# Kernel tuning notes

Hardware: AMD Instinct MI355X
Metric: run time of the kernel (lower is better)

## Reference

```python
import jax, jax.numpy as jnp
import numpy as np
from jax import lax

B, CIN, H, W = 2, 512, 64, 64
NCLS = 5
CI = CIN // 4      # inter_channels = 128
CQ = CI // 8       # PAM query/key channels = 16
EPS = 1e-5


def setup_inputs() -> dict:
    key = jax.random.key(0)
    it = iter(jax.random.split(key, 48))

    def nrm(shape, s=0.05):
        return jax.random.normal(next(it), shape, jnp.float32) * s

    def bn(c):
        w = jax.random.uniform(next(it), (c,), jnp.float32, 0.5, 1.5)
        b = nrm((c,))
        m = nrm((c,))
        v = jax.random.uniform(next(it), (c,), jnp.float32, 0.5, 1.5)
        return w, b, m, v

    inp = {}
    inp['x'] = jax.random.normal(next(it), (B, CIN, H, W), jnp.float32)
    inp['bn_a_w'], inp['bn_a_b'], inp['bn_a_m'], inp['bn_a_v'] = bn(CIN)
    inp['conv_a_w'] = nrm((CI, CIN, 3, 3))
    inp['bn_c_w'], inp['bn_c_b'], inp['bn_c_m'], inp['bn_c_v'] = bn(CIN)
    inp['conv_c_w'] = nrm((CI, CIN, 3, 3))
    inp['pam_q_w'] = nrm((CQ, CI)); inp['pam_q_b'] = nrm((CQ,))
    inp['pam_k_w'] = nrm((CQ, CI)); inp['pam_k_b'] = nrm((CQ,))
    inp['pam_v_w'] = nrm((CI, CI)); inp['pam_v_b'] = nrm((CI,))
    inp['pam_gamma'] = nrm((1,), 0.5)
    inp['cam_gamma'] = nrm((1,), 0.5)
    inp['bn_a1_w'], inp['bn_a1_b'], inp['bn_a1_m'], inp['bn_a1_v'] = bn(CI)
    inp['conv_a1_w'] = nrm((CIN, CI)); inp['conv_a1_b'] = nrm((CIN,))
    inp['bn_c1_w'], inp['bn_c1_b'], inp['bn_c1_m'], inp['bn_c1_v'] = bn(CI)
    inp['conv_c1_w'] = nrm((CIN, CI)); inp['conv_c1_b'] = nrm((CIN,))
    inp['out_a_w'] = nrm((NCLS, CIN)); inp['out_a_b'] = nrm((NCLS,))
    inp['out_c_w'] = nrm((NCLS, CIN)); inp['out_c_b'] = nrm((NCLS,))
    inp['out_f_w'] = nrm((NCLS, CIN)); inp['out_f_b'] = nrm((NCLS,))
    return inp


def _bn_relu(x, w, b, m, v):
    # eval-mode BatchNorm2d followed by ReLU
    scale = (w / jnp.sqrt(v + EPS))[None, :, None, None]
    shift = (b - m * w / jnp.sqrt(v + EPS))[None, :, None, None]
    return jax.nn.relu(x * scale + shift)


def _conv3(x, w):
    return lax.conv_general_dilated(x, w, (1, 1), 'SAME',
                                    dimension_numbers=('NCHW', 'OIHW', 'NCHW'))


def _conv1(x, w, b):
    # 1x1 conv as channel matmul
    return jnp.einsum('oi,bihw->bohw', w, x) + b[None, :, None, None]


def _pam(x, wq, bq, wk, bk, wv, bv, gamma):
    Bc, C, Hh, Ww = x.shape
    N = Hh * Ww
    q = _conv1(x, wq, bq).reshape(Bc, -1, N)   # [B,CQ,N]
    k = _conv1(x, wk, bk).reshape(Bc, -1, N)   # [B,CQ,N]
    v = _conv1(x, wv, bv).reshape(Bc, C, N)    # [B,C,N]
    energy = jnp.einsum('bcn,bcm->bnm', q, k)  # [B,N,N]
    attn = jax.nn.softmax(energy, axis=-1)
    out = jnp.einsum('bcm,bnm->bcn', v, attn).reshape(Bc, C, Hh, Ww)
    return gamma * out + x


def _cam(x, gamma):
    Bc, C, Hh, Ww = x.shape
    N = Hh * Ww
    f = x.reshape(Bc, C, N)
    energy = jnp.einsum('bcn,bdn->bcd', f, f)                    # [B,C,C]
    energy_new = jnp.max(energy, -1, keepdims=True) - energy
    attn = jax.nn.softmax(energy_new, axis=-1)
    out = jnp.einsum('bcd,bdn->bcn', attn, f).reshape(Bc, C, Hh, Ww)
    return gamma * out + x


def reference(x, bn_a_w, bn_a_b, bn_a_m, bn_a_v, conv_a_w,
              bn_c_w, bn_c_b, bn_c_m, bn_c_v, conv_c_w,
              pam_q_w, pam_q_b, pam_k_w, pam_k_b, pam_v_w, pam_v_b,
              pam_gamma, cam_gamma,
              bn_a1_w, bn_a1_b, bn_a1_m, bn_a1_v, conv_a1_w, conv_a1_b,
              bn_c1_w, bn_c1_b, bn_c1_m, bn_c1_v, conv_c1_w, conv_c1_b,
              out_a_w, out_a_b, out_c_w, out_c_b, out_f_w, out_f_b):
    # position-attention branch
    sa = _conv3(_bn_relu(x, bn_a_w, bn_a_b, bn_a_m, bn_a_v), conv_a_w)
    sa = _pam(sa, pam_q_w, pam_q_b, pam_k_w, pam_k_b, pam_v_w, pam_v_b, pam_gamma)
    sa = _conv1(_bn_relu(sa, bn_a1_w, bn_a1_b, bn_a1_m, bn_a1_v), conv_a1_w, conv_a1_b)
    # channel-attention branch
    sc = _conv3(_bn_relu(x, bn_c_w, bn_c_b, bn_c_m, bn_c_v), conv_c_w)
    sc = _cam(sc, cam_gamma)
    sc = _conv1(_bn_relu(sc, bn_c1_w, bn_c1_b, bn_c1_m, bn_c1_v), conv_c1_w, conv_c1_b)
    feat_fusion = sa + sc
    # dropout is identity at eval time
    sa_out = _conv1(sa, out_a_w, out_a_b)
    sc_out = _conv1(sc, out_c_w, out_c_b)
    sasc_out = _conv1(feat_fusion, out_f_w, out_f_b)
    return (feat_fusion, sasc_out, sa_out, sc_out)
```

## Files before the change

### kernel.cpp

```cpp
#include <hip/hip_runtime.h>

using u16 = unsigned short;
using short8 = __attribute__((ext_vector_type(8))) short;
using f32x4 = __attribute__((ext_vector_type(4))) float;

struct alignas(8) U16x4 { u16 x, y, z, w; };

__device__ __forceinline__ float bf2f(u16 u) {
  return __uint_as_float(((unsigned int)u) << 16);
}
__device__ __forceinline__ u16 f2bf(float f) {
  unsigned int u = __float_as_uint(f);
  unsigned int r = u + 0x7FFFu + ((u >> 16) & 1u);
  return (u16)(r >> 16);
}

__global__ void k_prep_w(const float* __restrict__ wa, const float* __restrict__ wc,
                         u16* __restrict__ Wb) {
  int idx = blockIdx.x * 256 + threadIdx.x;
  int j = idx & 7;
  int l = (idx >> 3) & 63;
  int ks = (idx >> 9) & 3;
  int rest = idx >> 11;
  int tap = rest % 9;
  int rest2 = rest / 9;
  int chunk = rest2 & 3;
  int mt = (rest2 >> 2) & 7;
  int br = rest2 >> 5;
  int co = mt * 16 + (l & 15);
  int ci = chunk * 128 + ks * 32 + (l >> 4) * 8 + j;
  const float* w = br ? wc : wa;
  Wb[idx] = f2bf(w[co * 4608 + ci * 9 + tap]);
}

__global__ void k_prep_w1(const float* __restrict__ wa, const float* __restrict__ wc,
                          u16* __restrict__ W1b) {
  int idx = blockIdx.x * 256 + threadIdx.x;
  int j = idx & 7;
  int l = (idx >> 3) & 63;
  int ks = (idx >> 9) & 3;
  int cot = (idx >> 11) & 31;
  int br = idx >> 16;
  int co = cot * 16 + (l & 15);
  int ci = ks * 32 + (l >> 4) * 8 + j;
  const float* w = br ? wc : wa;
  W1b[idx] = f2bf(w[co * 128 + ci]);
}

__global__ void k_prep_wqkv(const float* __restrict__ wq, const float* __restrict__ wk,
                            const float* __restrict__ wv, u16* __restrict__ Wq) {
  int idx = blockIdx.x * 256 + threadIdx.x;
  if (idx >= 20480) return;
  int j = idx & 7;
  int l = (idx >> 3) & 63;
  int ks = (idx >> 9) & 3;
  int cot = idx >> 11;
  int co = cot * 16 + (l & 15);
  int ci = ks * 32 + (l >> 4) * 8 + j;
  float w = co < 16 ? wq[co * 128 + ci]
          : (co < 32 ? wk[(co - 16) * 128 + ci] : wv[(co - 32) * 128 + ci]);
  Wq[idx] = f2bf(w);
}

__global__ __launch_bounds__(256) void k_bnrelu2t(const float* __restrict__ x,
    const float* __restrict__ wa, const float* __restrict__ ba,
    const float* __restrict__ ma, const float* __restrict__ va,
    const float* __restrict__ wc, const float* __restrict__ bc,
    const float* __restrict__ mc, const float* __restrict__ vc,
    u16* __restrict__ xa16, u16* __restrict__ xcb16) {
  __shared__ float sA[128], bA[128], sC[128], bC[128];
  __shared__ u16 ta[64 * 136], tc[64 * 136];
  int t = threadIdx.x;
  int h = blockIdx.x, b = blockIdx.y;
  int c0 = blockIdx.z * 128;
  if (t < 128) {
    int c = c0 + t;
    float s1 = wa[c] * rsqrtf(va[c] + 1e-5f);
    sA[t] = s1; bA[t] = ba[c] - ma[c] * s1;
    float s2 = wc[c] * rsqrtf(vc[c] + 1e-5f);
    sC[t] = s2; bC[t] = bc[c] - mc[c] * s2;
  }
  __syncthreads();
  const float* xb = x + ((size_t)b << 21) + (h << 6);
  u16* oa = xa16 + ((size_t)b << 21) + ((size_t)h << 15);
  u16* oc = xcb16 + ((size_t)b << 21) + ((size_t)h << 15);
  int w = t & 63, cg = t >> 6;
#pragma unroll
  for (int i = 0; i < 8; ++i) {
    int cl = cg * 4 + i * 16;
    int c = c0 + cl;
    const float* xp = xb + (size_t)c * 4096 + w;
    float v0 = xp[0], v1 = xp[4096], v2 = xp[8192], v3 = xp[12288];
    U16x4 pa, pc;
    pa.x = f2bf(fmaxf(fmaf(v0, sA[cl], bA[cl]), 0.f));
    pa.y = f2bf(fmaxf(fmaf(v1, sA[cl + 1], bA[cl + 1]), 0.f));
    pa.z = f2bf(fmaxf(fmaf(v2, sA[cl + 2], bA[cl + 2]), 0.f));
    pa.w = f2bf(fmaxf(fmaf(v3, sA[cl + 3], bA[cl + 3]), 0.f));
    pc.x = f2bf(fmaxf(fmaf(v0, sC[cl], bC[cl]), 0.f));
    pc.y = f2bf(fmaxf(fmaf(v1, sC[cl + 1], bC[cl + 1]), 0.f));
    pc.z = f2bf(fmaxf(fmaf(v2, sC[cl + 2], bC[cl + 2]), 0.f));
    pc.w = f2bf(fmaxf(fmaf(v3, sC[cl + 3], bC[cl + 3]), 0.f));
    *(U16x4*)(ta + w * 136 + cl) = pa;
    *(U16x4*)(tc + w * 136 + cl) = pc;
  }
  __syncthreads();
#pragma unroll
  for (int i = 0; i < 4; ++i) {
    int idx = t + i * 256;
    int ww = idx >> 4, c8 = (idx & 15) << 3;
    *(short8*)(oa + (size_t)ww * 512 + c0 + c8) = *(const short8*)(ta + ww * 136 + c8);
    *(short8*)(oc + (size_t)ww * 512 + c0 + c8) = *(const short8*)(tc + ww * 136 + c8);
  }
}

__global__ __launch_bounds__(256, 2) void k_conv3n(
    const u16* __restrict__ xa16, const u16* __restrict__ xcb16,
    const u16* __restrict__ Wb,
    float* __restrict__ sa0, float* __restrict__ sc0,
    u16* __restrict__ sa_nhwc, u16* __restrict__ sc16h, u16* __restrict__ sc16l) {
  __shared__ u16 xs[3 * 66 * 136];
  int t = threadIdx.x;
  int h = blockIdx.x;
  int z = blockIdx.y; int b = z & 1, br = z >> 1;
  int cosplit = blockIdx.z;
  const u16* xb = (br ? xcb16 : xa16) + ((size_t)b << 21);
  const u16* wb = Wb + (size_t)br * 589824;
  float* out = (br ? sc0 : sa0) + (((size_t)b * 128) << 12) + (h << 6);

  int lane = t & 63, wave = t >> 6;
  int mi = lane & 15, quad = lane >> 4;
  int mt = cosplit * 4 + wave;

  if (t < 96) {
    int dh = t >> 5, side = (t >> 4) & 1, c8 = t & 15;
    short8 z8 = {0, 0, 0, 0, 0, 0, 0, 0};
    *(short8*)(xs + (dh * 66 + side * 65) * 136 + c8 * 8) = z8;
  }

  f32x4 acc[4] = {};

  const u16* wlane = wb + lane * 8;
  const u16* bbase0 = xs + mi * 136 + quad * 8;

  for (int chunk = 0; chunk < 4; ++chunk) {
    int ci0 = chunk << 7;
    __syncthreads();
#pragma unroll
    for (int dh = 0; dh < 3; ++dh) {
      int hh = h + dh - 1;
      bool val = (hh >= 0) && (hh < 64);
      const u16* src = xb + (((size_t)hh << 6) << 9) + ci0;
#pragma unroll
      for (int i = 0; i < 4; ++i) {
        int idx = t + i * 256;
        int w = idx >> 4, c8 = (idx & 15) << 3;
        short8 v = {0, 0, 0, 0, 0, 0, 0, 0};
        if (val) v = *(const short8*)(src + ((size_t)w << 9) + c8);
        *(short8*)(xs + (dh * 66 + 1 + w) * 136 + c8) = v;
      }
    }
    __syncthreads();
    const u16* wchunk = wlane + (size_t)(mt * 4 + chunk) * 18432;
    short8 wreg[2][4];
#pragma unroll
    for (int ks = 0; ks < 4; ++ks)
      wreg[0][ks] = *(const short8*)(wchunk + ks * 512);
#pragma unroll
    for (int tap = 0; tap < 9; ++tap) {
      const int cb = tap & 1;
      if (tap < 8) {
        const u16* wn = wchunk + (tap + 1) * 2048;
#pragma unroll
        for (int ks = 0; ks < 4; ++ks)
          wreg[cb ^ 1][ks] = *(const short8*)(wn + ks * 512);
      }
      const int dh = tap / 3, dw = tap % 3;
      const u16* bp = bbase0 + (dh * 66 + dw) * 136;
#pragma unroll
      for (int ks = 0; ks < 4; ++ks) {
        short8 a = wreg[cb][ks];
#pragma unroll
        for (int nt = 0; nt < 4; ++nt) {
          short8 bf = *(const short8*)(bp + nt * 2176 + ks * 32);
          acc[nt] = __builtin_amdgcn_mfma_f32_16x16x32_bf16(a, bf, acc[nt], 0, 0, 0);
        }
      }
    }
  }
#pragma unroll
  for (int nt = 0; nt < 4; ++nt)
#pragma unroll
    for (int r = 0; r < 4; ++r) {
      int co = mt * 16 + quad * 4 + r;
      out[((size_t)co << 12) + nt * 16 + mi] = acc[nt][r];
    }
  if (br == 0) {
    u16* dstq = sa_nhwc + ((size_t)b << 19) + ((size_t)h << 6) * 128;
#pragma unroll
    for (int nt = 0; nt < 4; ++nt) {
      U16x4 v4;
      v4.x = f2bf(acc[nt][0]); v4.y = f2bf(acc[nt][1]);
      v4.z = f2bf(acc[nt][2]); v4.w = f2bf(acc[nt][3]);
      *(U16x4*)(dstq + (size_t)(nt * 16 + mi) * 128 + mt * 16 + quad * 4) = v4;
    }
  } else {
    u16* dh_ = sc16h + ((size_t)b << 19) + (h << 6);
    u16* dl_ = sc16l + ((size_t)b << 19) + (h << 6);
#pragma unroll
    for (int nt = 0; nt < 4; ++nt)
#pragma unroll
      for (int r = 0; r < 4; ++r) {
        int co = mt * 16 + quad * 4 + r;
        float xv = acc[nt][r];
        u16 hi = f2bf(xv);
        float lo = xv - bf2f(hi);
        size_t o = ((size_t)co << 12) + nt * 16 + mi;
        dh_[o] = hi;
        dl_[o] = f2bf(lo);
      }
  }
}

__global__ __launch_bounds__(256) void k_qkv(
    const u16* __restrict__ sa_nhwc, const u16* __restrict__ Wqkvb,
    const float* __restrict__ bq, const float* __restrict__ bk,
    const float* __restrict__ bv,
    float* __restrict__ qb, u16* __restrict__ k16t, u16* __restrict__ vt16) {
  __shared__ float bs[160];
  int t = threadIdx.x;
  int b = blockIdx.y, n0 = blockIdx.x * 128;
  if (t < 160) bs[t] = t < 16 ? bq[t] : (t < 32 ? bk[t - 16] : bv[t - 32]);
  __syncthreads();
  int lane = t & 63, wave = t >> 6;
  int mi = lane & 15, quad = lane >> 4;
  const u16* xb = sa_nhwc + ((size_t)b << 19) + (size_t)n0 * 128;
  const u16* wb = Wqkvb + lane * 8;
  f32x4 acc[2][10] = {};
  short8 bf[2][4];
#pragma unroll
  for (int ns = 0; ns < 2; ++ns) {
    int n = wave * 32 + ns * 16 + mi;
#pragma unroll
    for (int ks = 0; ks < 4; ++ks)
      bf[ns][ks] = *(const short8*)(xb + (size_t)n * 128 + ks * 32 + quad * 8);
  }
#pragma unroll
  for (int cot = 0; cot < 10; ++cot) {
    short8 a0 = *(const short8*)(wb + (size_t)(cot * 4 + 0) * 512);
    short8 a1 = *(const short8*)(wb + (size_t)(cot * 4 + 1) * 512);
    short8 a2 = *(const short8*)(wb + (size_t)(cot * 4 + 2) * 512);
    short8 a3 = *(const short8*)(wb + (size_t)(cot * 4 + 3) * 512);
#pragma unroll
    for (int ns = 0; ns < 2; ++ns) {
      acc[ns][cot] = __builtin_amdgcn_mfma_f32_16x16x32_bf16(a0, bf[ns][0], acc[ns][cot], 0, 0, 0);
      acc[ns][cot] = __builtin_amdgcn_mfma_f32_16x16x32_bf16(a1, bf[ns][1], acc[ns][cot], 0, 0, 0);
      acc[ns][cot] = __builtin_amdgcn_mfma_f32_16x16x32_bf16(a2, bf[ns][2], acc[ns][cot], 0, 0, 0);
      acc[ns][cot] = __builtin_amdgcn_mfma_f32_16x16x32_bf16(a3, bf[ns][3], acc[ns][cot], 0, 0, 0);
    }
  }
#pragma unroll
  for (int cot = 0; cot < 10; ++cot)
#pragma unroll
    for (int ns = 0; ns < 2; ++ns) {
      int n = n0 + wave * 32 + ns * 16 + mi;
      if (cot == 1) {
        u16 hv[4], lv[4];
#pragma unroll
        for (int r = 0; r < 4; ++r) {
          float v = acc[ns][1][r] + bs[16 + quad * 4 + r];
          u16 hi = f2bf(v);
          hv[r] = hi;
          lv[r] = f2bf(v - bf2f(hi));
        }
        u16* kd = k16t + (((size_t)b << 12) + n) * 32;
        U16x4 h4{hv[0], hv[1], hv[2], hv[3]};
        U16x4 l4{lv[0], lv[1], lv[2], lv[3]};
        *(U16x4*)(kd + quad * 4) = h4;
        *(U16x4*)(kd + 16 + quad * 4) = l4;
      } else {
#pragma unroll
        for (int r = 0; r < 4; ++r) {
          int co = cot * 16 + quad * 4 + r;
          float v = acc[ns][cot][r] + bs[co];
          if (co < 16) qb[((b * 16 + co) << 12) + n] = v;
          else vt16[((size_t)(b * 128 + co - 32) << 12) + n] = f2bf(v);
        }
      }
    }
}

__global__ __launch_bounds__(512, 4) void k_pam_pv(const float* __restrict__ qb,
    const u16* __restrict__ k16t, const u16* __restrict__ vt16,
    float* __restrict__ pvpart, float* __restrict__ pmax, float* __restrict__ psum) {
  constexpr int PSTR = 264;
  __shared__ u16 pL[32 * PSTR];
  __shared__ u16 qfh[32 * 16], qfl[32 * 16];
  __shared__ float wmx[8][2][16];
  __shared__ float wsm[8][2][16];
  int t = threadIdx.x;
  int b = blockIdx.y, n0 = blockIdx.x * 32;
  int mq = blockIdx.z;
  int mbeg = mq << 10;
  int lane = t & 63, wave = t >> 6;
  int mi = lane & 15, quad = lane >> 4;
  int c0 = wave * 16;
  {
    int ch = t & 15, nl = t >> 4;
    float qv = qb[((size_t)(b * 16 + ch) << 12) + n0 + nl];
    u16 hi = f2bf(qv);
    qfh[nl * 16 + ch] = hi;
    qfl[nl * 16 + ch] = f2bf(qv - bf2f(hi));
  }
  const u16* kp = k16t + (((size_t)b << 12) + mbeg) * 32;
  const u16* vb = vt16 + ((size_t)b * 128 << 12);
  f32x4 acc[2] = {};
  float mr0 = -1e30f, mr1 = -1e30f, ssum0 = 0.f, ssum1 = 0.f;
  __syncthreads();
  int qoff = (quad & 1) * 8;
  short8 bq1[2], bq2[2];
  bq1[0] = *(const short8*)(qfh + mi * 16 + qoff);
  bq1[1] = *(const short8*)(qfh + (16 + mi) * 16 + qoff);
  bq2[0] = *(const short8*)(qfl + mi * 16 + qoff);
  bq2[1] = *(const short8*)(qfl + (16 + mi) * 16 + qoff);
  size_t abase = (size_t)(wave * 32 + mi) * 32 + quad * 8;
  short8 a0c = *(const short8*)(kp + abase);
  short8 a1c = *(const short8*)(kp + abase + 512);
  for (int it = 0; it < 4; ++it) {
    int m0r = it << 8;
    short8 vreg[8];
#pragma unroll
    for (int ksl = 0; ksl < 8; ++ksl)
      vreg[ksl] = *(const short8*)(vb + ((size_t)(c0 + mi) << 12) + mbeg + m0r + ksl * 32 + quad * 8);
    short8 a0n, a1n;
    if (it < 3) {
      a0n = *(const short8*)(kp + (size_t)(it + 1) * 8192 + abase);
      a1n = *(const short8*)(kp + (size_t)(it + 1) * 8192 + abase + 512);
    }
    f32x4 e00 = {}, e01 = {}, e10 = {}, e11 = {};
    e00 = __builtin_amdgcn_mfma_f32_16x16x32_bf16(a0c, bq1[0], e00, 0, 0, 0);
    e00 = __builtin_amdgcn_mfma_f32_16x16x32_bf16(a0c, bq2[0], e00, 0, 0, 0);
    e01 = __builtin_amdgcn_mfma_f32_16x16x32_bf16(a0c, bq1[1], e01, 0, 0, 0);
    e01 = __builtin_amdgcn_mfma_f32_16x16x32_bf16(a0c, bq2[1], e01, 0, 0, 0);
    e10 = __builtin_amdgcn_mfma_f32_16x16x32_bf16(a1c, bq1[0], e10, 0, 0, 0);
    e10 = __builtin_amdgcn_mfma_f32_16x16x32_bf16(a1c, bq2[0], e10, 0, 0, 0);
    e11 = __builtin_amdgcn_mfma_f32_16x16x32_bf16(a1c, bq1[1], e11, 0, 0, 0);
    e11 = __builtin_amdgcn_mfma_f32_16x16x32_bf16(a1c, bq2[1], e11, 0, 0, 0);
    float lm0 = fmaxf(fmaxf(fmaxf(e00[0], e00[1]), fmaxf(e00[2], e00[3])),
                      fmaxf(fmaxf(e10[0], e10[1]), fmaxf(e10[2], e10[3])));
    float lm1 = fmaxf(fmaxf(fmaxf(e01[0], e01[1]), fmaxf(e01[2], e01[3])),
                      fmaxf(fmaxf(e11[0], e11[1]), fmaxf(e11[2], e11[3])));
    lm0 = fmaxf(lm0, __shfl_xor(lm0, 16)); lm0 = fmaxf(lm0, __shfl_xor(lm0, 32));
    lm1 = fmaxf(lm1, __shfl_xor(lm1, 16)); lm1 = fmaxf(lm1, __shfl_xor(lm1, 32));
    if (quad == 0) { wmx[wave][0][mi] = lm0; wmx[wave][1][mi] = lm1; }
    __syncthreads();
    float cm0 = wmx[0][0][mi], cm1 = wmx[0][1][mi];
#pragma unroll
    for (int w = 1; w < 8; ++w) {
      cm0 = fmaxf(cm0, wmx[w][0][mi]);
      cm1 = fmaxf(cm1, wmx[w][1][mi]);
    }
    float mn0 = fmaxf(mr0, cm0), mn1 = fmaxf(mr1, cm1);
    float rs0 = __expf(mr0 - mn0), rs1 = __expf(mr1 - mn1);
#pragma unroll
    for (int r = 0; r < 4; ++r) { acc[0][r] *= rs0; acc[1][r] *= rs1; }
    float p00[4], p10[4], p01[4], p11[4];
    float ls0 = 0.f, ls1 = 0.f;
#pragma unroll
    for (int j = 0; j < 4; ++j) {
      p00[j] = __expf(e00[j] - mn0); p10[j] = __expf(e10[j] - mn0);
      p01[j] = __expf(e01[j] - mn1); p11[j] = __expf(e11[j] - mn1);
      ls0 += p00[j] + p10[j];
      ls1 += p01[j] + p11[j];
    }
    ssum0 = ssum0 * rs0 + ls0;
    ssum1 = ssum1 * rs1 + ls1;
    mr0 = mn0; mr1 = mn1;
    u16* prow0 = pL + mi * PSTR + wave * 32 + quad * 4;
    u16* prow1 = pL + (16 + mi) * PSTR + wave * 32 + quad * 4;
    U16x4 p;
    p.x = f2bf(p00[0]); p.y = f2bf(p00[1]); p.z = f2bf(p00[2]); p.w = f2bf(p00[3]);
    *(U16x4*)(prow0) = p;
    p.x = f2bf(p10[0]); p.y = f2bf(p10[1]); p.z = f2bf(p10[2]); p.w = f2bf(p10[3]);
    *(U16x4*)(prow0 + 16) = p;
    p.x = f2bf(p01[0]); p.y = f2bf(p01[1]); p.z = f2bf(p01[2]); p.w = f2bf(p01[3]);
    *(U16x4*)(prow1) = p;
    p.x = f2bf(p11[0]); p.y = f2bf(p11[1]); p.z = f2bf(p11[2]); p.w = f2bf(p11[3]);
    *(U16x4*)(prow1 + 16) = p;
    __syncthreads();
#pragma unroll
    for (int ksl = 0; ksl < 8; ++ksl) {
      const u16* pb0 = pL + mi * PSTR + ksl * 32 + quad * 8;
      short8 b0 = *(const short8*)(pb0);
      short8 b1 = *(const short8*)(pb0 + 16 * PSTR);
      acc[0] = __builtin_amdgcn_mfma_f32_16x16x32_bf16(vreg[ksl], b0, acc[0], 0, 0, 0);
      acc[1] = __builtin_amdgcn_mfma_f32_16x16x32_bf16(vreg[ksl], b1, acc[1], 0, 0, 0);
    }
    a0c = a0n; a1c = a1n;
  }
  ssum0 += __shfl_xor(ssum0, 16); ssum0 += __shfl_xor(ssum0, 32);
  ssum1 += __shfl_xor(ssum1, 16); ssum1 += __shfl_xor(ssum1, 32);
  if (quad == 0) { wsm[wave][0][mi] = ssum0; wsm[wave][1][mi] = ssum1; }
  __syncthreads();
  if (t < 16) {
    float sA = 0.f, sB = 0.f;
#pragma unroll
    for (int w = 0; w < 8; ++w) { sA += wsm[w][0][t]; sB += wsm[w][1][t]; }
    size_t base = ((size_t)(mq * 2 + b) << 12) + n0;
    psum[base + t] = sA;
    psum[base + 16 + t] = sB;
    pmax[base + t] = mr0;
    pmax[base + 16 + t] = mr1;
  }
  float* dst = pvpart + (((size_t)(mq * 2 + b) * 128) << 12);
#pragma unroll
  for (int nh = 0; nh < 2; ++nh)
#pragma unroll
    for (int r = 0; r < 4; ++r) {
      int c = c0 + quad * 4 + r;
      dst[((size_t)c << 12) + n0 + nh * 16 + mi] = acc[nh][r];
    }
}

__global__ __launch_bounds__(512) void k_cam_energy_m(
    const u16* __restrict__ sc16h, const u16* __restrict__ sc16l,
    float* __restrict__ epart) {
  int t = threadIdx.x;
  int ti = blockIdx.x, kc = blockIdx.y, b = blockIdx.z;
  int lane = t & 63, wave = t >> 6;
  int mi = lane & 15, quad = lane >> 4;
  const u16* fh = sc16h + ((size_t)b << 19);
  const u16* fl = sc16l + ((size_t)b << 19);
  size_t ao = ((size_t)(ti * 16 + mi) << 12) + (kc << 9) + quad * 8;
  size_t bo = ((size_t)(wave * 16 + mi) << 12) + (kc << 9) + quad * 8;
  const u16* ah = fh + ao; const u16* al = fl + ao;
  const u16* bh = fh + bo; const u16* bl = fl + bo;
  f32x4 acc = {};
#pragma unroll
  for (int k = 0; k < 16; ++k) {
    short8 vah = *(const short8*)(ah + k * 32);
    short8 val = *(const short8*)(al + k * 32);
    short8 vbh = *(const short8*)(bh + k * 32);
    short8 vbl = *(const short8*)(bl + k * 32);
    acc = __builtin_amdgcn_mfma_f32_16x16x32_bf16(vah, vbh, acc, 0, 0, 0);
    acc = __builtin_amdgcn_mfma_f32_16x16x32_bf16(vah, vbl, acc, 0, 0, 0);
    acc = __builtin_amdgcn_mfma_f32_16x16x32_bf16(val, vbh, acc, 0, 0, 0);
  }
  float* ep = epart + (((size_t)(kc * 2 + b)) << 14);
#pragma unroll
  for (int r = 0; r < 4; ++r)
    ep[((ti * 16 + quad * 4 + r) << 7) + wave * 16 + mi] = acc[r];
}

__global__ void k_cam_softmax(const float* __restrict__ epart, float* __restrict__ attn) {
  int lane = threadIdx.x;
  int c = blockIdx.x, b = blockIdx.y;
  float e0 = 0.f, e1 = 0.f;
#pragma unroll
  for (int kc = 0; kc < 8; ++kc) {
    const float* ep = epart + (((size_t)(kc * 2 + b)) << 14) + (c << 7);
    e0 += ep[lane];
    e1 += ep[lane + 64];
  }
  float mn = fminf(e0, e1);
#pragma unroll
  for (int off = 32; off >= 1; off >>= 1) mn = fminf(mn, __shfl_xor(mn, off));
  float p0 = __expf(fminf(mn - e0, 0.f)), p1 = __expf(fminf(mn - e1, 0.f));
  float s = p0 + p1;
#pragma unroll
  for (int off = 32; off >= 1; off >>= 1) s += __shfl_xor(s, off);
  float inv = 1.f / s;
  float* a = attn + ((b * 128 + c) << 7);
  a[lane] = p0 * inv;
  a[lane + 64] = p1 * inv;
}

__global__ __launch_bounds__(256) void k_cam_out(const float* __restrict__ f,
    const float* __restrict__ attn, const float* __restrict__ gamma,
    float* __restrict__ sc1) {
  __shared__ float at2[128 * 8];
  int t = threadIdx.x;
  int b = blockIdx.z, c0 = blockIdx.y * 8;
  int n = blockIdx.x * 256 + t;
  for (int idx = t; idx < 1024; idx += 256) {
    int d = idx >> 3, cc = idx & 7;
    at2[idx] = attn[((b * 128 + c0 + cc) << 7) + d];
  }
  __syncthreads();
  float acc[8] = {};
  const float* fb = f + ((size_t)b * 128 << 12) + n;
  for (int d = 0; d < 128; ++d) {
    float fv = fb[d << 12];
    const float* ap = at2 + d * 8;
#pragma unroll
    for (int cc = 0; cc < 8; ++cc) acc[cc] = fmaf(ap[cc], fv, acc[cc]);
  }
  float g = gamma[0];
#pragma unroll
  for (int cc = 0; cc < 8; ++cc) {
    size_t o = ((size_t)(b * 128 + c0 + cc) << 12) + n;
    sc1[o] = fmaf(g, acc[cc], f[o]);
  }
}

__global__ __launch_bounds__(256, 2) void k_bout_m(
    const float* __restrict__ sa0, const float* __restrict__ pvpart,
    const float* __restrict__ pmax, const float* __restrict__ psum,
    const float* __restrict__ gamma,
    const float* __restrict__ sc1,
    const float* __restrict__ wa_, const float* __restrict__ ba_,
    const float* __restrict__ ma_, const float* __restrict__ va_,
    const float* __restrict__ wc_, const float* __restrict__ bc_,
    const float* __restrict__ mc_, const float* __restrict__ vc_,
    const u16* __restrict__ W1b, const float* __restrict__ Ba,
    const float* __restrict__ Bc,
    u16* __restrict__ sa2, u16* __restrict__ sc2) {
  __shared__ u16 xl[32 * 136];
  __shared__ float scl[128], shf[128];
  int t = threadIdx.x;
  int n0 = blockIdx.x * 32;
  int b = blockIdx.y, br = blockIdx.z;
  const float* bw = br ? wc_ : wa_;
  const float* bb = br ? bc_ : ba_;
  const float* bm = br ? mc_ : ma_;
  const float* bvv = br ? vc_ : va_;
  if (t < 128) {
    float s = bw[t] * rsqrtf(bvv[t] + 1e-5f);
    scl[t] = s;
    shf[t] = bb[t] - bm[t] * s;
  }
  __syncthreads();
  {
    int nl = t & 31, cio = t >> 5;
    const float* s0 = (br ? sc1 : sa0) + ((size_t)b * 128 << 12) + n0 + nl;
    const float* pq[4];
    float kq[4] = {};
    if (!br) {
      int n = n0 + nl;
      float m[4], s4[4];
#pragma unroll
      for (int q = 0; q < 4; ++q) {
        pq[q] = pvpart + (((size_t)(q * 2 + b) * 128) << 12) + n0 + nl;
        m[q] = pmax[((size_t)(q * 2 + b) << 12) + n];
        s4[q] = psum[((size_t)(q * 2 + b) << 12) + n];
      }
      float M = fmaxf(fmaxf(m[0], m[1]), fmaxf(m[2], m[3]));
      float den = 0.f;
#pragma unroll
      for (int q = 0; q < 4; ++q) { kq[q] = __expf(m[q] - M); den = fmaf(kq[q], s4[q], den); }
      float inv = gamma[0] / den;
#pragma unroll
      for (int q = 0; q < 4; ++q) kq[q] *= inv;
    }
#pragma unroll
    for (int half = 0; half < 2; ++half) {
      short8 v;
#pragma unroll
      for (int i = 0; i < 8; ++i) {
        int ci = cio * 16 + half * 8 + i;
        float xv = s0[(size_t)ci << 12];
        if (!br) {
          size_t po = (size_t)ci << 12;
          xv += kq[0] * pq[0][po] + kq[1] * pq[1][po]
              + kq[2] * pq[2][po] + kq[3] * pq[3][po];
        }
        v[i] = (short)f2bf(fmaxf(fmaf(xv, scl[ci], shf[ci]), 0.f));
      }
      *(short8*)(xl + nl * 136 + cio * 16 + half * 8) = v;
    }
  }
  __syncthreads();
  int lane = t & 63, wave = t >> 6;
  int mi = lane & 15, quad = lane >> 4;
  const u16* wb = W1b + (size_t)br * 65536 + lane * 8;
  f32x4 acc[8][2] = {};
#pragma unroll
  for (int ks = 0; ks < 4; ++ks) {
    short8 b0 = *(const short8*)(xl + mi * 136 + ks * 32 + quad * 8);
    short8 b1 = *(const short8*)(xl + (16 + mi) * 136 + ks * 32 + quad * 8);
#pragma unroll
    for (int ct = 0; ct < 8; ++ct) {
      int cot = wave * 8 + ct;
      short8 a = *(const short8*)(wb + ((size_t)(cot * 4 + ks) << 9));
      acc[ct][0] = __builtin_amdgcn_mfma_f32_16x16x32_bf16(a, b0, acc[ct][0], 0, 0, 0);
      acc[ct][1] = __builtin_amdgcn_mfma_f32_16x16x32_bf16(a, b1, acc[ct][1], 0, 0, 0);
    }
  }
  const float* Bs = br ? Bc : Ba;
  u16* dst = br ? sc2 : sa2;
#pragma unroll
  for (int ct = 0; ct < 8; ++ct)
#pragma unroll
    for (int nh = 0; nh < 2; ++nh)
#pragma unroll
      for (int r = 0; r < 4; ++r) {
        int co = (wave * 8 + ct) * 16 + quad * 4 + r;
        dst[((size_t)(b * 512 + co) << 12) + n0 + nh * 16 + mi] =
            f2bf(acc[ct][nh][r] + Bs[co]);
      }
}

__global__ __launch_bounds__(256) void k_heads2(const u16* __restrict__ sa2,
    const u16* __restrict__ sc2,
    const float* __restrict__ wf, const float* __restrict__ wa, const float* __restrict__ wc,
    const float* __restrict__ bfb, const float* __restrict__ bab,
    const float* __restrict__ bcb,
    float* __restrict__ outFusion, float* __restrict__ outCls) {
  __shared__ float lw[3 * 5 * 512];
  __shared__ float hs[16][15][16];
  int t = threadIdx.x;
  int b = blockIdx.y, n0 = blockIdx.x * 16;
  for (int idx = t; idx < 7680; idx += 256) {
    int arr = idx / 2560, rest = idx - arr * 2560;
    int cls = rest >> 9, co = rest & 511;
    const float* w = arr == 0 ? wf : (arr == 1 ? wa : wc);
    lw[idx] = w[cls * 512 + co];
  }
  __syncthreads();
  int nl = t & 15, ck = t >> 4;
  float acc[15] = {};
  for (int co = ck * 32; co < ck * 32 + 32; ++co) {
    size_t o = ((size_t)(b * 512 + co) << 12) + n0 + nl;
    float a = bf2f(sa2[o]), c = bf2f(sc2[o]);
    float s = a + c;
    outFusion[o] = s;
    const float* lf = lw + co;
#pragma unroll
    for (int cls = 0; cls < 5; ++cls) {
      acc[cls]      = fmaf(lf[cls * 512], s, acc[cls]);
      acc[5 + cls]  = fmaf(lf[2560 + cls * 512], a, acc[5 + cls]);
      acc[10 + cls] = fmaf(lf[5120 + cls * 512], c, acc[10 + cls]);
    }
  }
#pragma unroll
  for (int k = 0; k < 15; ++k) hs[ck][k][nl] = acc[k];
  __syncthreads();
  for (int idx = t; idx < 240; idx += 256) {
    int k = idx >> 4, nl2 = idx & 15;
    float s = 0.f;
#pragma unroll
    for (int c8 = 0; c8 < 16; ++c8) s += hs[c8][k][nl2];
    int arr = k / 5, cls = k - arr * 5;
    float bias = arr == 0 ? bfb[cls] : (arr == 1 ? bab[cls] : bcb[cls]);
    outCls[arr * 40960 + ((b * 5 + cls) << 12) + n0 + nl2] = s + bias;
  }
}

extern "C" void kernel_launch(void* const* d_in, const int* in_sizes, int n_in,
                              void* d_out, int out_size, void* d_ws, size_t ws_size,
                              hipStream_t stream) {
  (void)in_sizes; (void)n_in; (void)out_size; (void)ws_size;
  const float* x      = (const float*)d_in[0];
  const float* bnaw   = (const float*)d_in[1];
  const float* bnab   = (const float*)d_in[2];
  const float* bnam   = (const float*)d_in[3];
  const float* bnav   = (const float*)d_in[4];
  const float* convaw = (const float*)d_in[5];
  const float* bncw   = (const float*)d_in[6];
  const float* bncb   = (const float*)d_in[7];
  const float* bncm   = (const float*)d_in[8];
  const float* bncv   = (const float*)d_in[9];
  const float* convcw = (const float*)d_in[10];
  const float* pqw    = (const float*)d_in[11];
  const float* pqb    = (const float*)d_in[12];
  const float* pkw    = (const float*)d_in[13];
  const float* pkb    = (const float*)d_in[14];
  const float* pvw    = (const float*)d_in[15];
  const float* pvb    = (const float*)d_in[16];
  const float* pgam   = (const float*)d_in[17];
  const float* cgam   = (const float*)d_in[18];
  const float* bna1w  = (const float*)d_in[19];
  const float* bna1b  = (const float*)d_in[20];
  const float* bna1m  = (const float*)d_in[21];
  const float* bna1v  = (const float*)d_in[22];
  const float* conva1w = (const float*)d_in[23];
  const float* conva1b = (const float*)d_in[24];
  const float* bnc1w  = (const float*)d_in[25];
  const float* bnc1b  = (const float*)d_in[26];
  const float* bnc1m  = (const float*)d_in[27];
  const float* bnc1v  = (const float*)d_in[28];
  const float* convc1w = (const float*)d_in[29];
  const float* convc1b = (const float*)d_in[30];
  const float* outaw  = (const float*)d_in[31];
  const float* outab  = (const float*)d_in[32];
  const float* outcw  = (const float*)d_in[33];
  const float* outcb  = (const float*)d_in[34];
  const float* outfw  = (const float*)d_in[35];
  const float* outfb  = (const float*)d_in[36];

  char* wsb = (char*)d_ws;
  size_t off = 0;
  auto take = [&](size_t bytes) -> void* {
    void* p = wsb + off;
    off += (bytes + 255) & ~(size_t)255;
    return p;
  };
  u16*   Wb    = (u16*)take((size_t)2 * 128 * 9 * 512 * 2);
  u16*   W1b   = (u16*)take((size_t)2 * 512 * 128 * 2);
  u16*   Wqkvb = (u16*)take((size_t)160 * 128 * 2);
  u16*   xa16  = (u16*)take((size_t)2 * 512 * 4096 * 2);
  u16*   xcb16 = (u16*)take((size_t)2 * 512 * 4096 * 2);
  float* sa0   = (float*)take((size_t)2 * 128 * 4096 * 4);
  float* sc0   = (float*)take((size_t)2 * 128 * 4096 * 4);
  u16*   sa_nhwc = (u16*)take((size_t)2 * 4096 * 128 * 2);
  u16*   sc16h = (u16*)take((size_t)2 * 128 * 4096 * 2);
  u16*   sc16l = (u16*)take((size_t)2 * 128 * 4096 * 2);
  float* qb    = (float*)take((size_t)2 * 16 * 4096 * 4);
  u16*   k16t  = (u16*)take((size_t)2 * 4096 * 32 * 2);
  u16*   vt16  = (u16*)take((size_t)2 * 128 * 4096 * 2);
  float* pvpart = (float*)take((size_t)4 * 2 * 128 * 4096 * 4);
  float* pmax  = (float*)take((size_t)4 * 2 * 4096 * 4);
  float* psum  = (float*)take((size_t)4 * 2 * 4096 * 4);
  float* sc1   = (float*)take((size_t)2 * 128 * 4096 * 4);
  float* epart = (float*)take((size_t)8 * 2 * 128 * 128 * 4);
  float* attn  = (float*)take((size_t)2 * 128 * 128 * 4);
  u16*   sa2   = (u16*)take((size_t)2 * 512 * 4096 * 2);
  u16*   sc2   = (u16*)take((size_t)2 * 512 * 4096 * 2);

  float* outF = (float*)d_out;
  float* outCls = outF + (size_t)2 * 512 * 4096;

  k_prep_w<<<4608, 256, 0, stream>>>(convaw, convcw, Wb);
  k_prep_w1<<<512, 256, 0, stream>>>(conva1w, convc1w, W1b);
  k_prep_wqkv<<<80, 256, 0, stream>>>(pqw, pkw, pvw, Wqkvb);
  k_bnrelu2t<<<dim3(64, 2, 4), 256, 0, stream>>>(x, bnaw, bnab, bnam, bnav,
                                                 bncw, bncb, bncm, bncv, xa16, xcb16);
  k_conv3n<<<dim3(64, 4, 2), 256, 0, stream>>>(xa16, xcb16, Wb, sa0, sc0,
                                               sa_nhwc, sc16h, sc16l);
  k_qkv<<<dim3(32, 2), 256, 0, stream>>>(sa_nhwc, Wqkvb, pqb, pkb, pvb,
                                         qb, k16t, vt16);
  k_pam_pv<<<dim3(128, 2, 4), 512, 0, stream>>>(qb, k16t, vt16, pvpart, pmax, psum);
  k_cam_energy_m<<<dim3(8, 8, 2), 512, 0, stream>>>(sc16h, sc16l, epart);
  k_cam_softmax<<<dim3(128, 2), 64, 0, stream>>>(epart, attn);
  k_cam_out<<<dim3(16, 16, 2), 256, 0, stream>>>(sc0, attn, cgam, sc1);
  k_bout_m<<<dim3(128, 2, 2), 256, 0, stream>>>(sa0, pvpart, pmax, psum, pgam, sc1,
      bna1w, bna1b, bna1m, bna1v, bnc1w, bnc1b, bnc1m, bnc1v,
      W1b, conva1b, convc1b, sa2, sc2);
  k_heads2<<<dim3(256, 2), 256, 0, stream>>>(sa2, sc2, outfw, outaw, outcw,
                                             outfb, outab, outcb, outF, outCls);
}
```

Before: 292.3 us.

## Make PAM flash-attention waves independent with 8-way key split and lazy rescale

Restructures the PAM attention kernel so each wave owns a 512-key slice and all 128 value channels. This removes the block-wide max reduction and both __syncthreads per iteration, and the P tile now goes through per-wave LDS. Rescaling of the accumulators is skipped unless the running max grows, checked with a wave ballot. In exchange the kernel holds 64 accumulator registers, runs fewer waves per block, and the split count rises from 4 to 8, which doubles the partial output buffer that the combine kernel must read.

Measured after the change: 292.3 us. No clear change (-0.0%).

```diff
diff --git a/kernel.cpp b/kernel.cpp
--- a/kernel.cpp
+++ b/kernel.cpp
@@ -289,80 +289,72 @@
     }
 }
 
-__global__ __launch_bounds__(512, 4) void k_pam_pv(const float* __restrict__ qb,
+__global__ __launch_bounds__(256, 2) void k_pam_pv(const float* __restrict__ qb,
     const u16* __restrict__ k16t, const u16* __restrict__ vt16,
     float* __restrict__ pvpart, float* __restrict__ pmax, float* __restrict__ psum) {
-  constexpr int PSTR = 264;
-  __shared__ u16 pL[32 * PSTR];
+  __shared__ u16 pL[4][32 * 36];
   __shared__ u16 qfh[32 * 16], qfl[32 * 16];
-  __shared__ float wmx[8][2][16];
-  __shared__ float wsm[8][2][16];
   int t = threadIdx.x;
   int b = blockIdx.y, n0 = blockIdx.x * 32;
-  int mq = blockIdx.z;
-  int mbeg = mq << 10;
   int lane = t & 63, wave = t >> 6;
   int mi = lane & 15, quad = lane >> 4;
-  int c0 = wave * 16;
-  {
-    int ch = t & 15, nl = t >> 4;
+  for (int i = t; i < 512; i += 256) {
+    int ch = i & 15, nl = i >> 4;
     float qv = qb[((size_t)(b * 16 + ch) << 12) + n0 + nl];
     u16 hi = f2bf(qv);
     qfh[nl * 16 + ch] = hi;
     qfl[nl * 16 + ch] = f2bf(qv - bf2f(hi));
   }
+  __syncthreads();
+  int p = blockIdx.z * 4 + wave;
+  int mbeg = p << 9;
   const u16* kp = k16t + (((size_t)b << 12) + mbeg) * 32;
-  const u16* vb = vt16 + ((size_t)b * 128 << 12);
-  f32x4 acc[2] = {};
-  float mr0 = -1e30f, mr1 = -1e30f, ssum0 = 0.f, ssum1 = 0.f;
-  __syncthreads();
+  const u16* vb = vt16 + ((size_t)b * 128 << 12) + mbeg;
+  u16* pw = pL[wave];
   int qoff = (quad & 1) * 8;
   short8 bq1[2], bq2[2];
   bq1[0] = *(const short8*)(qfh + mi * 16 + qoff);
   bq1[1] = *(const short8*)(qfh + (16 + mi) * 16 + qoff);
   bq2[0] = *(const short8*)(qfl + mi * 16 + qoff);
   bq2[1] = *(const short8*)(qfl + (16 + mi) * 16 + qoff);
-  size_t abase = (size_t)(wave * 32 + mi) * 32 + quad * 8;
-  short8 a0c = *(const short8*)(kp + abase);
-  short8 a1c = *(const short8*)(kp + abase + 512);
-  for (int it = 0; it < 4; ++it) {
-    int m0r = it << 8;
+  f32x4 acc[8][2] = {};
+  float mr0 = -1e30f, mr1 = -1e30f, ssum0 = 0.f, ssum1 = 0.f;
+  for (int it = 0; it < 16; ++it) {
+    int m0 = it << 5;
     short8 vreg[8];
 #pragma unroll
-    for (int ksl = 0; ksl < 8; ++ksl)
-      vreg[ksl] = *(const short8*)(vb + ((size_t)(c0 + mi) << 12) + mbeg + m0r + ksl * 32 + quad * 8);
-    short8 a0n, a1n;
-    if (it < 3) {
-      a0n = *(const short8*)(kp + (size_t)(it + 1) * 8192 + abase);
-      a1n = *(const short8*)(kp + (size_t)(it + 1) * 8192 + abase + 512);
-    }
+    for (int ct = 0; ct < 8; ++ct)
+      vreg[ct] = *(const short8*)(vb + ((size_t)(ct * 16 + mi) << 12) + m0 + quad * 8);
+    const u16* ka = kp + (size_t)m0 * 32;
+    short8 a0 = *(const short8*)(ka + mi * 32 + quad * 8);
+    short8 a1 = *(const short8*)(ka + (16 + mi) * 32 + quad * 8);
     f32x4 e00 = {}, e01 = {}, e10 = {}, e11 = {};
-    e00 = __builtin_amdgcn_mfma_f32_16x16x32_bf16(a0c, bq1[0], e00, 0, 0, 0);
-    e00 = __builtin_amdgcn_mfma_f32_16x16x32_bf16(a0c, bq2[0], e00, 0, 0, 0);
-    e01 = __builtin_amdgcn_mfma_f32_16x16x32_bf16(a0c, bq1[1], e01, 0, 0, 0);
-    e01 = __builtin_amdgcn_mfma_f32_16x16x32_bf16(a0c, bq2[1], e01, 0, 0, 0);
-    e10 = __builtin_amdgcn_mfma_f32_16x16x32_bf16(a1c, bq1[0], e10, 0, 0, 0);
-    e10 = __builtin_amdgcn_mfma_f32_16x16x32_bf16(a1c, bq2[0], e10, 0, 0, 0);
-    e11 = __builtin_amdgcn_mfma_f32_16x16x32_bf16(a1c, bq1[1], e11, 0, 0, 0);
-    e11 = __builtin_amdgcn_mfma_f32_16x16x32_bf16(a1c, bq2[1], e11, 0, 0, 0);
+    e00 = __builtin_amdgcn_mfma_f32_16x16x32_bf16(a0, bq1[0], e00, 0, 0, 0);
+    e00 = __builtin_amdgcn_mfma_f32_16x16x32_bf16(a0, bq2[0], e00, 0, 0, 0);
+    e01 = __builtin_amdgcn_mfma_f32_16x16x32_bf16(a0, bq1[1], e01, 0, 0, 0);
+    e01 = __builtin_amdgcn_mfma_f32_16x16x32_bf16(a0, bq2[1], e01, 0, 0, 0);
+    e10 = __builtin_amdgcn_mfma_f32_16x16x32_bf16(a1, bq1[0], e10, 0, 0, 0);
+    e10 = __builtin_amdgcn_mfma_f32_16x16x32_bf16(a1, bq2[0], e10, 0, 0, 0);
+    e11 = __builtin_amdgcn_mfma_f32_16x16x32_bf16(a1, bq1[1], e11, 0, 0, 0);
+    e11 = __builtin_amdgcn_mfma_f32_16x16x32_bf16(a1, bq2[1], e11, 0, 0, 0);
     float lm0 = fmaxf(fmaxf(fmaxf(e00[0], e00[1]), fmaxf(e00[2], e00[3])),
                       fmaxf(fmaxf(e10[0], e10[1]), fmaxf(e10[2], e10[3])));
     float lm1 = fmaxf(fmaxf(fmaxf(e01[0], e01[1]), fmaxf(e01[2], e01[3])),
                       fmaxf(fmaxf(e11[0], e11[1]), fmaxf(e11[2], e11[3])));
     lm0 = fmaxf(lm0, __shfl_xor(lm0, 16)); lm0 = fmaxf(lm0, __shfl_xor(lm0, 32));
     lm1 = fmaxf(lm1, __shfl_xor(lm1, 16)); lm1 = fmaxf(lm1, __shfl_xor(lm1, 32));
-    if (quad == 0) { wmx[wave][0][mi] = lm0; wmx[wave][1][mi] = lm1; }
-    __syncthreads();
-    float cm0 = wmx[0][0][mi], cm1 = wmx[0][1][mi];
-#pragma unroll
-    for (int w = 1; w < 8; ++w) {
-      cm0 = fmaxf(cm0, wmx[w][0][mi]);
-      cm1 = fmaxf(cm1, wmx[w][1][mi]);
-    }
-    float mn0 = fmaxf(mr0, cm0), mn1 = fmaxf(mr1, cm1);
-    float rs0 = __expf(mr0 - mn0), rs1 = __expf(mr1 - mn1);
-#pragma unroll
-    for (int r = 0; r < 4; ++r) { acc[0][r] *= rs0; acc[1][r] *= rs1; }
+    float mn0 = mr0, mn1 = mr1;
+    bool need = (__ballot(lm0 > mr0) | __ballot(lm1 > mr1)) != 0ull;
+    if (need) {
+      mn0 = fmaxf(mr0, lm0); mn1 = fmaxf(mr1, lm1);
+      float rs0 = __expf(mr0 - mn0), rs1 = __expf(mr1 - mn1);
+#pragma unroll
+      for (int ct = 0; ct < 8; ++ct)
+#pragma unroll
+        for (int r = 0; r < 4; ++r) { acc[ct][0][r] *= rs0; acc[ct][1][r] *= rs1; }
+      ssum0 *= rs0; ssum1 *= rs1;
+      mr0 = mn0; mr1 = mn1;
+    }
     float p00[4], p10[4], p01[4], p11[4];
     float ls0 = 0.f, ls1 = 0.f;
 #pragma unroll
@@ -372,53 +364,44 @@
       ls0 += p00[j] + p10[j];
       ls1 += p01[j] + p11[j];
     }
-    ssum0 = ssum0 * rs0 + ls0;
-    ssum1 = ssum1 * rs1 + ls1;
-    mr0 = mn0; mr1 = mn1;
-    u16* prow0 = pL + mi * PSTR + wave * 32 + quad * 4;
-    u16* prow1 = pL + (16 + mi) * PSTR + wave * 32 + quad * 4;
-    U16x4 p;
-    p.x = f2bf(p00[0]); p.y = f2bf(p00[1]); p.z = f2bf(p00[2]); p.w = f2bf(p00[3]);
-    *(U16x4*)(prow0) = p;
-    p.x = f2bf(p10[0]); p.y = f2bf(p10[1]); p.z = f2bf(p10[2]); p.w = f2bf(p10[3]);
-    *(U16x4*)(prow0 + 16) = p;
-    p.x = f2bf(p01[0]); p.y = f2bf(p01[1]); p.z = f2bf(p01[2]); p.w = f2bf(p01[3]);
-    *(U16x4*)(prow1) = p;
-    p.x = f2bf(p11[0]); p.y = f2bf(p11[1]); p.z = f2bf(p11[2]); p.w = f2bf(p11[3]);
-    *(U16x4*)(prow1 + 16) = p;
-    __syncthreads();
-#pragma unroll
-    for (int ksl = 0; ksl < 8; ++ksl) {
-      const u16* pb0 = pL + mi * PSTR + ksl * 32 + quad * 8;
-      short8 b0 = *(const short8*)(pb0);
-      short8 b1 = *(const short8*)(pb0 + 16 * PSTR);
-      acc[0] = __builtin_amdgcn_mfma_f32_16x16x32_bf16(vreg[ksl], b0, acc[0], 0, 0, 0);
-      acc[1] = __builtin_amdgcn_mfma_f32_16x16x32_bf16(vreg[ksl], b1, acc[1], 0, 0, 0);
-    }
-    a0c = a0n; a1c = a1n;
+    ssum0 += ls0;
+    ssum1 += ls1;
+    U16x4 pk;
+    pk.x = f2bf(p00[0]); pk.y = f2bf(p00[1]); pk.z = f2bf(p00[2]); pk.w = f2bf(p00[3]);
+    *(U16x4*)(pw + mi * 36 + quad * 4) = pk;
+    pk.x = f2bf(p10[0]); pk.y = f2bf(p10[1]); pk.z = f2bf(p10[2]); pk.w = f2bf(p10[3]);
+    *(U16x4*)(pw + mi * 36 + 16 + quad * 4) = pk;
+    pk.x = f2bf(p01[0]); pk.y = f2bf(p01[1]); pk.z = f2bf(p01[2]); pk.w = f2bf(p01[3]);
+    *(U16x4*)(pw + (16 + mi) * 36 + quad * 4) = pk;
+    pk.x = f2bf(p11[0]); pk.y = f2bf(p11[1]); pk.z = f2bf(p11[2]); pk.w = f2bf(p11[3]);
+    *(U16x4*)(pw + (16 + mi) * 36 + 16 + quad * 4) = pk;
+    short8 b0 = *(const short8*)(pw + mi * 36 + quad * 8);
+    short8 b1 = *(const short8*)(pw + (16 + mi) * 36 + quad * 8);
+#pragma unroll
+    for (int ct = 0; ct < 8; ++ct) {
+      acc[ct][0] = __builtin_amdgcn_mfma_f32_16x16x32_bf16(vreg[ct], b0, acc[ct][0], 0, 0, 0);
+      acc[ct][1] = __builtin_amdgcn_mfma_f32_16x16x32_bf16(vreg[ct], b1, acc[ct][1], 0, 0, 0);
+    }
   }
   ssum0 += __shfl_xor(ssum0, 16); ssum0 += __shfl_xor(ssum0, 32);
   ssum1 += __shfl_xor(ssum1, 16); ssum1 += __shfl_xor(ssum1, 32);
-  if (quad == 0) { wsm[wave][0][mi] = ssum0; wsm[wave][1][mi] = ssum1; }
-  __syncthreads();
-  if (t < 16) {
-    float sA = 0.f, sB = 0.f;
-#pragma unroll
-    for (int w = 0; w < 8; ++w) { sA += wsm[w][0][t]; sB += wsm[w][1][t]; }
-    size_t base = ((size_t)(mq * 2 + b) << 12) + n0;
-    psum[base + t] = sA;
-    psum[base + 16 + t] = sB;
-    pmax[base + t] = mr0;
-    pmax[base + 16 + t] = mr1;
-  }
-  float* dst = pvpart + (((size_t)(mq * 2 + b) * 128) << 12);
-#pragma unroll
-  for (int nh = 0; nh < 2; ++nh)
-#pragma unroll
-    for (int r = 0; r < 4; ++r) {
-      int c = c0 + quad * 4 + r;
-      dst[((size_t)c << 12) + n0 + nh * 16 + mi] = acc[nh][r];
-    }
+  if (lane < 16) {
+    size_t base = ((size_t)(p * 2 + b) << 12) + n0;
+    psum[base + mi] = ssum0;
+    psum[base + 16 + mi] = ssum1;
+    pmax[base + mi] = mr0;
+    pmax[base + 16 + mi] = mr1;
+  }
+  float* dst = pvpart + (((size_t)(p * 2 + b) * 128) << 12);
+#pragma unroll
+  for (int ct = 0; ct < 8; ++ct)
+#pragma unroll
+    for (int nt = 0; nt < 2; ++nt)
+#pragma unroll
+      for (int r = 0; r < 4; ++r) {
+        int c = ct * 16 + quad * 4 + r;
+        dst[((size_t)c << 12) + n0 + nt * 16 + mi] = acc[ct][nt][r];
+      }
 }
 
 __global__ __launch_bounds__(512) void k_cam_energy_m(
@@ -532,24 +515,26 @@
   {
     int nl = t & 31, cio = t >> 5;
     const float* s0 = (br ? sc1 : sa0) + ((size_t)b * 128 << 12) + n0 + nl;
-    const float* pq[4];
-    float kq[4] = {};
+    const float* pq[8];
+    float kq[8] = {};
     if (!br) {
       int n = n0 + nl;
-      float m[4], s4[4];
-#pragma unroll
-      for (int q = 0; q < 4; ++q) {
+      float m[8], s8[8];
+#pragma unroll
+      for (int q = 0; q < 8; ++q) {
         pq[q] = pvpart + (((size_t)(q * 2 + b) * 128) << 12) + n0 + nl;
         m[q] = pmax[((size_t)(q * 2 + b) << 12) + n];
-        s4[q] = psum[((size_t)(q * 2 + b) << 12) + n];
-      }
-      float M = fmaxf(fmaxf(m[0], m[1]), fmaxf(m[2], m[3]));
+        s8[q] = psum[((size_t)(q * 2 + b) << 12) + n];
+      }
+      float M = m[0];
+#pragma unroll
+      for (int q = 1; q < 8; ++q) M = fmaxf(M, m[q]);
       float den = 0.f;
 #pragma unroll
-      for (int q = 0; q < 4; ++q) { kq[q] = __expf(m[q] - M); den = fmaf(kq[q], s4[q], den); }
+      for (int q = 0; q < 8; ++q) { kq[q] = __expf(m[q] - M); den = fmaf(kq[q], s8[q], den); }
       float inv = gamma[0] / den;
 #pragma unroll
-      for (int q = 0; q < 4; ++q) kq[q] *= inv;
+      for (int q = 0; q < 8; ++q) kq[q] *= inv;
     }
 #pragma unroll
     for (int half = 0; half < 2; ++half) {
@@ -560,8 +545,10 @@
         float xv = s0[(size_t)ci << 12];
         if (!br) {
           size_t po = (size_t)ci << 12;
-          xv += kq[0] * pq[0][po] + kq[1] * pq[1][po]
-              + kq[2] * pq[2][po] + kq[3] * pq[3][po];
+          float pv = 0.f;
+#pragma unroll
+          for (int q = 0; q < 8; ++q) pv = fmaf(kq[q], pq[q][po], pv);
+          xv += pv;
         }
         v[i] = (short)f2bf(fmaxf(fmaf(xv, scl[ci], shf[ci]), 0.f));
       }
@@ -707,9 +694,9 @@
   float* qb    = (float*)take((size_t)2 * 16 * 4096 * 4);
   u16*   k16t  = (u16*)take((size_t)2 * 4096 * 32 * 2);
   u16*   vt16  = (u16*)take((size_t)2 * 128 * 4096 * 2);
-  float* pvpart = (float*)take((size_t)4 * 2 * 128 * 4096 * 4);
-  float* pmax  = (float*)take((size_t)4 * 2 * 4096 * 4);
-  float* psum  = (float*)take((size_t)4 * 2 * 4096 * 4);
+  float* pvpart = (float*)take((size_t)8 * 2 * 128 * 4096 * 4);
+  float* pmax  = (float*)take((size_t)8 * 2 * 4096 * 4);
+  float* psum  = (float*)take((size_t)8 * 2 * 4096 * 4);
   float* sc1   = (float*)take((size_t)2 * 128 * 4096 * 4);
   float* epart = (float*)take((size_t)8 * 2 * 128 * 128 * 4);
   float* attn  = (float*)take((size_t)2 * 128 * 128 * 4);
@@ -728,7 +715,7 @@
                                                sa_nhwc, sc16h, sc16l);
   k_qkv<<<dim3(32, 2), 256, 0, stream>>>(sa_nhwc, Wqkvb, pqb, pkb, pvb,
                                          qb, k16t, vt16);
-  k_pam_pv<<<dim3(128, 2, 4), 512, 0, stream>>>(qb, k16t, vt16, pvpart, pmax, psum);
+  k_pam_pv<<<dim3(128, 2, 2), 256, 0, stream>>>(qb, k16t, vt16, pvpart, pmax, psum);
   k_cam_energy_m<<<dim3(8, 8, 2), 512, 0, stream>>>(sc16h, sc16l, epart);
   k_cam_softmax<<<dim3(128, 2), 64, 0, stream>>>(epart, attn);
   k_cam_out<<<dim3(16, 16, 2), 256, 0, stream>>>(sc0, attn, cgam, sc1);
```
